# Performance work log

Hardware: AMD Instinct MI355X
Metric: run time of the kernel (lower is better)

The kernel has to match this reference:

```python
import jax, jax.numpy as jnp
import numpy as np

DIM = 768
DEPTH = 6
HEADS = 12
DIM_HEAD = 64
INNER = HEADS * DIM_HEAD  # 768
MLP = DIM * 4
B, N = 4, 2048
EPS = 1e-5


def setup_inputs() -> dict:
    key = jax.random.key(0)
    ks = jax.random.split(key, 8)
    s = lambda *sh: 0.02
    inp = {
        "x": jax.random.normal(ks[0], (B, N, DIM), dtype=jnp.float32),
        "ln1_g": jnp.ones((DEPTH, DIM), jnp.float32),
        "ln1_b": jnp.zeros((DEPTH, DIM), jnp.float32),
        "wqkv": jax.random.normal(ks[1], (DEPTH, DIM, 3 * INNER), jnp.float32) * 0.02,
        "wout": jax.random.normal(ks[2], (DEPTH, INNER, DIM), jnp.float32) * 0.02,
        "ln2_g": jnp.ones((DEPTH, DIM), jnp.float32),
        "ln2_b": jnp.zeros((DEPTH, DIM), jnp.float32),
        "w1": jax.random.normal(ks[3], (DEPTH, DIM, MLP), jnp.float32) * 0.02,
        "b1": jnp.zeros((DEPTH, MLP), jnp.float32),
        "w2": jax.random.normal(ks[4], (DEPTH, MLP, DIM), jnp.float32) * 0.02,
        "b2": jnp.zeros((DEPTH, DIM), jnp.float32),
        "fn_g": jnp.ones((DIM,), jnp.float32),
        "fn_b": jnp.zeros((DIM,), jnp.float32),
    }
    return inp


def layer_norm(x, g, b):
    mu = jnp.mean(x, axis=-1, keepdims=True)
    var = jnp.mean(jnp.square(x - mu), axis=-1, keepdims=True)
    return (x - mu) * jax.lax.rsqrt(var + EPS) * g + b


def attention(x, wqkv, wout):
    # x: [b, n, dim]
    qkv = x @ wqkv  # [b, n, 3*inner]
    q, k, v = jnp.split(qkv, 3, axis=-1)
    split_heads = lambda t: t.reshape(t.shape[0], t.shape[1], HEADS, DIM_HEAD).transpose(0, 2, 1, 3)
    q, k, v = split_heads(q), split_heads(k), split_heads(v)  # [b, h, n, d]
    scale = DIM_HEAD ** -0.5
    dots = jnp.einsum("bhnd,bhmd->bhnm", q, k) * scale
    attn = jax.nn.softmax(dots, axis=-1)
    out = jnp.einsum("bhnm,bhmd->bhnd", attn, v)
    out = out.transpose(0, 2, 1, 3).reshape(x.shape[0], x.shape[1], INNER)
    return out @ wout


def feed_forward(x, w1, b1, w2, b2):
    h = jax.nn.gelu(x @ w1 + b1, approximate=False)
    return h @ w2 + b2


def reference(x, ln1_g, ln1_b, wqkv, wout, ln2_g, ln2_b, w1, b1, w2, b2, fn_g, fn_b):
    for i in range(DEPTH):
        x = x + attention(layer_norm(x, ln1_g[i], ln1_b[i]), wqkv[i], wout[i])
        x = x + feed_forward(layer_norm(x, ln2_g[i], ln2_b[i]), w1[i], b1[i], w2[i], b2[i])
    return layer_norm(x, fn_g, fn_b)
```

## Files before the change

### kernel.cpp

```cpp
#include <hip/hip_runtime.h>
#include <hip/hip_bf16.h>

typedef unsigned short ushort_t;
typedef unsigned int uint_t;
typedef __bf16 bf16x8 __attribute__((ext_vector_type(8)));
typedef float floatx4 __attribute__((ext_vector_type(4)));
typedef float floatx16 __attribute__((ext_vector_type(16)));

#define DIM 768
#define DEPTH 6
#define HEADS 12
#define DH 64
#define MLP_DIM 3072
#define BATCH 4
#define SEQ 2048
#define MTOK (BATCH * SEQ)
#define QKV3 (3 * DIM)

__device__ __forceinline__ float bf2f(unsigned u) {
    return __uint_as_float((u & 0xffffu) << 16);
}
__device__ __forceinline__ ushort_t f2bf(float f) {
    unsigned x = __float_as_uint(f);
    return (ushort_t)((x + 0x7FFFu + ((x >> 16) & 1u)) >> 16);
}
__device__ __forceinline__ void load_lds16(const void* g, void* l) {
    __builtin_amdgcn_global_load_lds((const __attribute__((address_space(1))) uint_t*)g,
                                     (__attribute__((address_space(3))) uint_t*)l, 16, 0, 0);
}
__device__ __forceinline__ uint_t cvt_pk_bf16(float lo, float hi) {
    uint_t r;
    asm("v_cvt_pk_bf16_f32 %0, %1, %2" : "=v"(r) : "v"(lo), "v"(hi));
    return r;
}
__device__ __forceinline__ float exp2_raw(float x) {
#if __has_builtin(__builtin_amdgcn_exp2f)
    return __builtin_amdgcn_exp2f(x);
#else
    return exp2f(x);
#endif
}

__global__ __launch_bounds__(256) void transpose_cvt(const float* __restrict__ in,
                                                     ushort_t* __restrict__ out,
                                                     int K, int N) {
    __shared__ float tile[32][33];
    const int d = blockIdx.z;
    in += (size_t)d * K * N;
    out += (size_t)d * K * N;
    const int n0 = blockIdx.x * 32, k0 = blockIdx.y * 32;
    for (int i = threadIdx.y; i < 32; i += 8) {
        tile[i][threadIdx.x] = in[(size_t)(k0 + i) * N + n0 + threadIdx.x];
    }
    __syncthreads();
    for (int i = threadIdx.y; i < 32; i += 8) {
        out[(size_t)(n0 + i) * K + k0 + threadIdx.x] = f2bf(tile[threadIdx.x][i]);
    }
}

template <bool OUTBF>
__global__ __launch_bounds__(256) void layernorm_k(const float* __restrict__ x,
                                                   const float* __restrict__ g,
                                                   const float* __restrict__ bta,
                                                   void* __restrict__ out) {
    const int row = blockIdx.x, t = threadIdx.x;
    const float* xr = x + (size_t)row * DIM;
    float v0 = xr[t], v1 = xr[t + 256], v2 = xr[t + 512];
    float s = v0 + v1 + v2;
    float sq = v0 * v0 + v1 * v1 + v2 * v2;
#pragma unroll
    for (int off = 32; off > 0; off >>= 1) {
        s += __shfl_down(s, off, 64);
        sq += __shfl_down(sq, off, 64);
    }
    __shared__ float ss[4], ssq[4];
    const int w = t >> 6;
    if ((t & 63) == 0) { ss[w] = s; ssq[w] = sq; }
    __syncthreads();
    s = ss[0] + ss[1] + ss[2] + ss[3];
    sq = ssq[0] + ssq[1] + ssq[2] + ssq[3];
    const float mean = s * (1.0f / DIM);
    const float var = sq * (1.0f / DIM) - mean * mean;
    const float rstd = rsqrtf(var + 1e-5f);
    float y0 = (v0 - mean) * rstd * g[t] + bta[t];
    float y1 = (v1 - mean) * rstd * g[t + 256] + bta[t + 256];
    float y2 = (v2 - mean) * rstd * g[t + 512] + bta[t + 512];
    if (OUTBF) {
        ushort_t* o = (ushort_t*)out + (size_t)row * DIM;
        o[t] = f2bf(y0); o[t + 256] = f2bf(y1); o[t + 512] = f2bf(y2);
    } else {
        float* o = (float*)out + (size_t)row * DIM;
        o[t] = y0; o[t + 256] = y1; o[t + 512] = y2;
    }
}

template <bool BIAS, bool GELU, bool RES, bool OUTBF>
__global__ __launch_bounds__(256) void gemm_bt(const ushort_t* __restrict__ A,
                                               const ushort_t* __restrict__ Bt,
                                               const float* __restrict__ bias,
                                               const float* __restrict__ resid,
                                               void* __restrict__ Cout,
                                               int M, int N, int K) {
    __shared__ ushort_t lds_a[128 * 32];
    __shared__ ushort_t lds_b[128 * 32];
    const int t = threadIdx.x;
    const int lane = t & 63, w = t >> 6;
    const int wm = w >> 1, wn = w & 1;
    const int bm = blockIdx.y * 128, bn = blockIdx.x * 128;

    floatx4 acc[4][4];
#pragma unroll
    for (int i = 0; i < 4; i++)
#pragma unroll
        for (int j = 0; j < 4; j++) acc[i][j] = (floatx4)0.0f;

    const int arow = t >> 2;
    const int asw = ((t & 3) ^ ((t >> 3) & 3)) * 8;
    const ushort_t* Abase = A + (size_t)(bm + arow) * K + asw;
    const ushort_t* Bbase = Bt + (size_t)(bn + arow) * K + asw;
    ushort_t* la = lds_a + t * 8;
    ushort_t* lb = lds_b + t * 8;

    const int mrow = wm * 64 + (lane & 15);
    const int nrow = wn * 64 + (lane & 15);
    const int quad = lane >> 4;
    const int kca = (quad ^ ((mrow >> 1) & 3)) * 8;
    const int kcb = (quad ^ ((nrow >> 1) & 3)) * 8;

    for (int k0 = 0; k0 < K; k0 += 32) {
        __syncthreads();
        load_lds16(Abase + k0, la);
        load_lds16(Abase + (size_t)64 * K + k0, la + 64 * 32);
        load_lds16(Bbase + k0, lb);
        load_lds16(Bbase + (size_t)64 * K + k0, lb + 64 * 32);
        __syncthreads();

        bf16x8 af[4], bfr[4];
#pragma unroll
        for (int i = 0; i < 4; i++) {
            af[i] = *(const bf16x8*)(lds_a + (mrow + i * 16) * 32 + kca);
            bfr[i] = *(const bf16x8*)(lds_b + (nrow + i * 16) * 32 + kcb);
        }
#pragma unroll
        for (int i = 0; i < 4; i++)
#pragma unroll
            for (int j = 0; j < 4; j++)
                acc[i][j] = __builtin_amdgcn_mfma_f32_16x16x32_bf16(af[i], bfr[j], acc[i][j], 0, 0, 0);
    }

    const int colq = lane & 15, rq = lane >> 4;
#pragma unroll
    for (int j = 0; j < 4; j++) {
        const int col = bn + wn * 64 + j * 16 + colq;
        const float bv = BIAS ? bias[col] : 0.0f;
#pragma unroll
        for (int i = 0; i < 4; i++) {
#pragma unroll
            for (int r = 0; r < 4; r++) {
                const int row = bm + wm * 64 + i * 16 + rq * 4 + r;
                float v = acc[i][j][r] + bv;
                if (GELU) v = 0.5f * v * (1.0f + erff(v * 0.70710678118654752f));
                const size_t idx = (size_t)row * N + col;
                if (RES) v += resid[idx];
                if (OUTBF) ((ushort_t*)Cout)[idx] = f2bf(v);
                else ((float*)Cout)[idx] = v;
            }
        }
    }
}

#define TSTR 66

__global__ __launch_bounds__(256) void v_transpose(const ushort_t* __restrict__ qkv,
                                                   ushort_t* __restrict__ vt) {
    __shared__ ushort_t tile[64 * TSTR];
    const int t = threadIdx.x;
    const int tk = blockIdx.x, h = blockIdx.y, b = blockIdx.z;
#pragma unroll
    for (int rep = 0; rep < 2; rep++) {
        const int s = t + rep * 256;
        const int row = s >> 3, uo = (s & 7) * 8;
        *(uint4*)(tile + row * TSTR + uo) =
            *(const uint4*)(qkv + (size_t)(b * SEQ + tk * 64 + row) * QKV3 + 2 * DIM + h * DH + uo);
    }
    __syncthreads();
#pragma unroll
    for (int rep = 0; rep < 2; rep++) {
        const int s = t + rep * 256;
        const int d = s >> 3, to = (s & 7) * 8;
        ushort_t tmp[8];
#pragma unroll
        for (int j = 0; j < 8; j++) tmp[j] = tile[(to + j) * TSTR + d];
        *(uint4*)(vt + ((size_t)(b * HEADS + h) * DH + d) * SEQ + tk * 64 + to) = *(uint4*)tmp;
    }
}

#define SC2 0.18033688011112042f

__global__ __launch_bounds__(256, 3) void attn_mfma(const ushort_t* __restrict__ qkv,
                                                    const ushort_t* __restrict__ vt,
                                                    ushort_t* __restrict__ outp) {
    __shared__ ushort_t lds_k[2][64 * 64];
    __shared__ ushort_t lds_vt[2][64 * 64];

    const int t = threadIdx.x;
    const int lane = t & 63, w = t >> 6;
    const int h = blockIdx.y, b = blockIdx.z;
    const int q0 = blockIdx.x * 128 + w * 32;
    const int l31 = lane & 31, hi = lane >> 5;

    bf16x8 qf[4];
#pragma unroll
    for (int dc = 0; dc < 4; dc++) {
        const uint4 raw = *(const uint4*)(qkv + (size_t)(b * SEQ + q0 + l31) * QKV3 +
                                          h * DH + dc * 16 + hi * 8);
        const uint_t rr[4] = {raw.x, raw.y, raw.z, raw.w};
        union { ushort_t u[8]; bf16x8 v; } qq;
#pragma unroll
        for (int e = 0; e < 4; e++) {
            qq.u[2 * e] = f2bf(bf2f(rr[e]) * SC2);
            qq.u[2 * e + 1] = f2bf(bf2f(rr[e] >> 16) * SC2);
        }
        qf[dc] = qq.v;
    }

    union { ushort_t u[8]; bf16x8 v; } onef;
#pragma unroll
    for (int e = 0; e < 8; e++) onef.u[e] = 0x3F80;

    floatx16 o[2];
    o[0] = (floatx16)0.0f; o[1] = (floatx16)0.0f;
    floatx16 osum = (floatx16)0.0f;

    const int srow = w * 16 + (lane >> 3);
    const int sg = ((lane & 7) ^ ((lane >> 3) & 7)) * 8;
    const ushort_t* kgbase = qkv + (size_t)(b * SEQ + srow) * QKV3 + DIM + h * DH + sg;
    const ushort_t* vgbase = vt + ((size_t)(b * HEADS + h) * DH + srow) * SEQ + sg;

    auto stage = [&](int kt) {
        const int bsel = kt & 1;
        ushort_t* ldk = (ushort_t*)lds_k[bsel] + w * 16 * 64;
        ushort_t* ldv = (ushort_t*)lds_vt[bsel] + w * 16 * 64;
        const ushort_t* kg = kgbase + (size_t)kt * 64 * QKV3;
        const ushort_t* vg = vgbase + kt * 64;
        load_lds16(kg, ldk);
        load_lds16(kg + (size_t)8 * QKV3, ldk + 8 * 64);
        load_lds16(vg, ldv);
        load_lds16(vg + (size_t)8 * SEQ, ldv + 8 * 64);
    };

    stage(0);
    for (int kt = 0; kt < SEQ / 64; kt++) {
        __syncthreads();
        stage((kt + 1) & (SEQ / 64 - 1));
        const ushort_t* ldk = lds_k[kt & 1];
        const ushort_t* ldv = lds_vt[kt & 1];

#pragma unroll
        for (int kt2 = 0; kt2 < 2; kt2++) {
            const int krow = kt2 * 32 + l31;
            const int ksw = krow & 7;
            floatx16 s = (floatx16)0.0f;
#pragma unroll
            for (int dc = 0; dc < 4; dc++) {
                const bf16x8 kf = *(const bf16x8*)(ldk + krow * 64 + ((dc * 2 + hi) ^ ksw) * 8);
                s = __builtin_amdgcn_mfma_f32_32x32x16_bf16(kf, qf[dc], s, 0, 0, 0);
            }

            bf16x8 vfr[2][2];
#pragma unroll
            for (int kc = 0; kc < 2; kc++)
#pragma unroll
                for (int dhalf = 0; dhalf < 2; dhalf++) {
                    const int vrow = dhalf * 32 + l31;
                    const int kcg = kt2 * 2 + kc;
                    vfr[kc][dhalf] =
                        *(const bf16x8*)(ldv + vrow * 64 + (((kcg * 2 + hi) ^ (vrow & 7)) * 8));
                }

            float p[16];
#pragma unroll
            for (int r = 0; r < 16; r++) p[r] = exp2_raw(s[r]);

#pragma unroll
            for (int kc = 0; kc < 2; kc++) {
                uint_t da = cvt_pk_bf16(p[kc * 8 + 0], p[kc * 8 + 1]);
                uint_t db = cvt_pk_bf16(p[kc * 8 + 2], p[kc * 8 + 3]);
                uint_t dcq = cvt_pk_bf16(p[kc * 8 + 4], p[kc * 8 + 5]);
                uint_t dd = cvt_pk_bf16(p[kc * 8 + 6], p[kc * 8 + 7]);
                asm volatile("v_permlane32_swap_b32 %0, %1" : "+v"(da), "+v"(dcq));
                asm volatile("v_permlane32_swap_b32 %0, %1" : "+v"(db), "+v"(dd));
                union { uint_t u[4]; bf16x8 v; } pa;
                pa.u[0] = da; pa.u[1] = db; pa.u[2] = dcq; pa.u[3] = dd;
                osum = __builtin_amdgcn_mfma_f32_32x32x16_bf16(pa.v, onef.v, osum, 0, 0, 0);
                o[0] = __builtin_amdgcn_mfma_f32_32x32x16_bf16(pa.v, vfr[kc][0], o[0], 0, 0, 0);
                o[1] = __builtin_amdgcn_mfma_f32_32x32x16_bf16(pa.v, vfr[kc][1], o[1], 0, 0, 0);
            }
        }
    }

#pragma unroll
    for (int r = 0; r < 16; r++) {
        const int ql = (r & 3) + 8 * (r >> 2) + 4 * hi;
        const float inv = 1.0f / osum[r];
        const size_t rowbase = (size_t)(b * SEQ + q0 + ql) * DIM + h * DH;
        outp[rowbase + l31] = f2bf(o[0][r] * inv);
        outp[rowbase + 32 + l31] = f2bf(o[1][r] * inv);
    }
}

extern "C" void kernel_launch(void* const* d_in, const int* in_sizes, int n_in,
                              void* d_out, int out_size, void* d_ws, size_t ws_size,
                              hipStream_t stream) {
    const float* x_in  = (const float*)d_in[0];
    const float* ln1_g = (const float*)d_in[1];
    const float* ln1_b = (const float*)d_in[2];
    const float* wqkv  = (const float*)d_in[3];
    const float* wout  = (const float*)d_in[4];
    const float* ln2_g = (const float*)d_in[5];
    const float* ln2_b = (const float*)d_in[6];
    const float* w1    = (const float*)d_in[7];
    const float* b1    = (const float*)d_in[8];
    const float* w2    = (const float*)d_in[9];
    const float* b2    = (const float*)d_in[10];
    const float* fn_g  = (const float*)d_in[11];
    const float* fn_b  = (const float*)d_in[12];

    char* ws = (char*)d_ws;
    size_t off = 0;
    auto alloc = [&](size_t bytes) -> char* {
        char* p = ws + off;
        off = (off + bytes + 255) & ~(size_t)255;
        return p;
    };
    ushort_t* wT_qkv = (ushort_t*)alloc((size_t)DEPTH * QKV3 * DIM * 2);
    ushort_t* wT_out = (ushort_t*)alloc((size_t)DEPTH * DIM * DIM * 2);
    ushort_t* wT_1   = (ushort_t*)alloc((size_t)DEPTH * MLP_DIM * DIM * 2);
    ushort_t* wT_2   = (ushort_t*)alloc((size_t)DEPTH * DIM * MLP_DIM * 2);
    float*    xbuf   = (float*)alloc((size_t)MTOK * DIM * 4);
    ushort_t* lnbuf  = (ushort_t*)alloc((size_t)MTOK * DIM * 2);
    ushort_t* qkvbuf = (ushort_t*)alloc((size_t)MTOK * QKV3 * 2);
    ushort_t* attnbuf= (ushort_t*)alloc((size_t)MTOK * DIM * 2);
    ushort_t* hbuf   = (ushort_t*)alloc((size_t)MTOK * MLP_DIM * 2);
    ushort_t* vtbuf  = hbuf;
    (void)ws_size; (void)in_sizes; (void)n_in; (void)out_size;

    transpose_cvt<<<dim3(QKV3 / 32, DIM / 32, DEPTH), dim3(32, 8), 0, stream>>>(wqkv, wT_qkv, DIM, QKV3);
    transpose_cvt<<<dim3(DIM / 32, DIM / 32, DEPTH), dim3(32, 8), 0, stream>>>(wout, wT_out, DIM, DIM);
    transpose_cvt<<<dim3(MLP_DIM / 32, DIM / 32, DEPTH), dim3(32, 8), 0, stream>>>(w1, wT_1, DIM, MLP_DIM);
    transpose_cvt<<<dim3(DIM / 32, MLP_DIM / 32, DEPTH), dim3(32, 8), 0, stream>>>(w2, wT_2, MLP_DIM, DIM);

    hipMemcpyAsync(xbuf, x_in, (size_t)MTOK * DIM * sizeof(float), hipMemcpyDeviceToDevice, stream);

    for (int i = 0; i < DEPTH; i++) {
        layernorm_k<true><<<MTOK, 256, 0, stream>>>(xbuf, ln1_g + i * DIM, ln1_b + i * DIM, lnbuf);
        gemm_bt<false, false, false, true><<<dim3(QKV3 / 128, MTOK / 128), 256, 0, stream>>>(
            lnbuf, wT_qkv + (size_t)i * QKV3 * DIM, nullptr, nullptr, qkvbuf, MTOK, QKV3, DIM);
        v_transpose<<<dim3(SEQ / 64, HEADS, BATCH), 256, 0, stream>>>(qkvbuf, vtbuf);
        attn_mfma<<<dim3(SEQ / 128, HEADS, BATCH), 256, 0, stream>>>(qkvbuf, vtbuf, attnbuf);
        gemm_bt<false, false, true, false><<<dim3(DIM / 128, MTOK / 128), 256, 0, stream>>>(
            attnbuf, wT_out + (size_t)i * DIM * DIM, nullptr, xbuf, xbuf, MTOK, DIM, DIM);
        layernorm_k<true><<<MTOK, 256, 0, stream>>>(xbuf, ln2_g + i * DIM, ln2_b + i * DIM, lnbuf);
        gemm_bt<true, true, false, true><<<dim3(MLP_DIM / 128, MTOK / 128), 256, 0, stream>>>(
            lnbuf, wT_1 + (size_t)i * MLP_DIM * DIM, b1 + (size_t)i * MLP_DIM, nullptr, hbuf, MTOK, MLP_DIM, DIM);
        gemm_bt<true, false, true, false><<<dim3(DIM / 128, MTOK / 128), 256, 0, stream>>>(
            hbuf, wT_2 + (size_t)i * DIM * MLP_DIM, b2 + (size_t)i * DIM, xbuf, xbuf, MTOK, DIM, MLP_DIM);
    }
    layernorm_k<false><<<MTOK, 256, 0, stream>>>(xbuf, fn_g, fn_b, (float*)d_out);
}
```

Baseline: 2.136 ms.

## Double-buffer GEMM LDS tiles and remap workgroup ids across XCDs

The bf16 MFMA GEMM now keeps two LDS buffers for the A and B tiles. It issues the global-to-LDS load for the next K step before computing on the current one, with a single barrier per iteration, so memory latency can overlap with MFMA work. It also remaps the linear workgroup id in groups of 8 so that neighbouring tiles land on the same XCD and share L2. The cost is twice the LDS use per block, which may lower occupancy, and the overlap only happens if load_lds16 is asynchronous.

New measurement: 2.013 ms. -5.8%, faster.

```diff
diff --git a/kernel.cpp b/kernel.cpp
--- a/kernel.cpp
+++ b/kernel.cpp
@@ -101,12 +101,17 @@
                                                const float* __restrict__ resid,
                                                void* __restrict__ Cout,
                                                int M, int N, int K) {
-    __shared__ ushort_t lds_a[128 * 32];
-    __shared__ ushort_t lds_b[128 * 32];
+    __shared__ ushort_t lds_a[2][128 * 32];
+    __shared__ ushort_t lds_b[2][128 * 32];
     const int t = threadIdx.x;
     const int lane = t & 63, w = t >> 6;
     const int wm = w >> 1, wn = w & 1;
-    const int bm = blockIdx.y * 128, bn = blockIdx.x * 128;
+
+    const int nwg = gridDim.x * gridDim.y;
+    int bid = blockIdx.y * gridDim.x + blockIdx.x;
+    bid = (bid & 7) * (nwg >> 3) + (bid >> 3);
+    const int bx = bid % gridDim.x, by = bid / gridDim.x;
+    const int bm = by * 128, bn = bx * 128;
 
     floatx4 acc[4][4];
 #pragma unroll
@@ -118,8 +123,6 @@
     const int asw = ((t & 3) ^ ((t >> 3) & 3)) * 8;
     const ushort_t* Abase = A + (size_t)(bm + arow) * K + asw;
     const ushort_t* Bbase = Bt + (size_t)(bn + arow) * K + asw;
-    ushort_t* la = lds_a + t * 8;
-    ushort_t* lb = lds_b + t * 8;
 
     const int mrow = wm * 64 + (lane & 15);
     const int nrow = wn * 64 + (lane & 15);
@@ -127,19 +130,30 @@
     const int kca = (quad ^ ((mrow >> 1) & 3)) * 8;
     const int kcb = (quad ^ ((nrow >> 1) & 3)) * 8;
 
-    for (int k0 = 0; k0 < K; k0 += 32) {
-        __syncthreads();
+    const int nk = K >> 5;
+    auto stage = [&](int kt) {
+        const int bsel = kt & 1;
+        const int k0 = kt * 32;
+        ushort_t* la = lds_a[bsel] + t * 8;
+        ushort_t* lb = lds_b[bsel] + t * 8;
         load_lds16(Abase + k0, la);
         load_lds16(Abase + (size_t)64 * K + k0, la + 64 * 32);
         load_lds16(Bbase + k0, lb);
         load_lds16(Bbase + (size_t)64 * K + k0, lb + 64 * 32);
+    };
+
+    stage(0);
+    for (int kt = 0; kt < nk; kt++) {
         __syncthreads();
+        if (kt + 1 < nk) stage(kt + 1);
+        const ushort_t* la = lds_a[kt & 1];
+        const ushort_t* lb = lds_b[kt & 1];
 
         bf16x8 af[4], bfr[4];
 #pragma unroll
         for (int i = 0; i < 4; i++) {
-            af[i] = *(const bf16x8*)(lds_a + (mrow + i * 16) * 32 + kca);
-            bfr[i] = *(const bf16x8*)(lds_b + (nrow + i * 16) * 32 + kcb);
+            af[i] = *(const bf16x8*)(la + (mrow + i * 16) * 32 + kca);
+            bfr[i] = *(const bf16x8*)(lb + (nrow + i * 16) * 32 + kcb);
         }
 #pragma unroll
         for (int i = 0; i < 4; i++)
```
